# Kernel optimization log

Measured on AMD Instinct MI355X. Metric: run time of the kernel, lower is better.

## Reference

```python
import jax, jax.numpy as jnp
import numpy as np

B, R, T = 128, 36, 40
E, V, H1, H2, PH, VOC = 1024, 2048, 1024, 1024, 256, 10000


def _lstm_cell(x, h, c, Wi, Wh, b):
    # torch gate order: i, f, g, o
    g = x @ Wi.T + h @ Wh.T + b
    i, f, gg, o = jnp.split(g, 4, axis=-1)
    c_new = jax.nn.sigmoid(f) * c + jax.nn.sigmoid(i) * jnp.tanh(gg)
    h_new = jax.nn.sigmoid(o) * jnp.tanh(c_new)
    return h_new, c_new


def setup_inputs() -> dict:
    key = jax.random.key(0)
    ks = jax.random.split(key, 20)
    s = 0.05
    Vmat = jax.random.normal(ks[0], (B, R, V), jnp.float32)
    enc_features = jax.random.normal(ks[1], (B, V), jnp.float32)
    union_vfeats = jax.random.normal(ks[2], (B, V), jnp.float32)
    captions = jax.random.randint(ks[3], (B, T), 0, VOC, jnp.int32)
    lengths = jax.random.randint(ks[4], (B,), 1, T + 1, jnp.int32)
    lengths = jnp.sort(lengths)[::-1].at[0].set(T)  # sorted descending, max first
    embed_W = jax.random.normal(ks[5], (VOC, E), jnp.float32) * s
    Wi1 = jax.random.normal(ks[6], (4 * H1, H2 + V + E), jnp.float32) * s
    Wh1 = jax.random.normal(ks[7], (4 * H1, H1), jnp.float32) * s
    b1 = jax.random.normal(ks[8], (4 * H1,), jnp.float32) * s
    Wi2 = jax.random.normal(ks[9], (4 * H2, H1 + V), jnp.float32) * s
    Wh2 = jax.random.normal(ks[10], (4 * H2, H2), jnp.float32) * s
    b2 = jax.random.normal(ks[11], (4 * H2,), jnp.float32) * s
    Wva = jax.random.normal(ks[12], (PH, V), jnp.float32) * s
    bva = jax.random.normal(ks[13], (PH,), jnp.float32) * s
    Wha = jax.random.normal(ks[14], (PH, H1), jnp.float32) * s
    bha = jax.random.normal(ks[15], (PH,), jnp.float32) * s
    wa = jax.random.normal(ks[16], (PH,), jnp.float32) * s
    ba = jax.random.normal(ks[17], (), jnp.float32) * s
    Wl = jax.random.normal(ks[18], (VOC, H2), jnp.float32) * s
    bl = jax.random.normal(ks[19], (VOC,), jnp.float32) * s
    return dict(Vmat=Vmat, enc_features=enc_features, union_vfeats=union_vfeats,
                captions=captions, lengths=lengths, embed_W=embed_W,
                Wi1=Wi1, Wh1=Wh1, b1=b1, Wi2=Wi2, Wh2=Wh2, b2=b2,
                Wva=Wva, bva=bva, Wha=Wha, bha=bha, wa=wa, ba=ba, Wl=Wl, bl=bl)


def reference(Vmat, enc_features, union_vfeats, captions, lengths, embed_W,
              Wi1, Wh1, b1, Wi2, Wh2, b2, Wva, bva, Wha, bha, wa, ba, Wl, bl):
    embeddings = embed_W[captions]                      # [B, T, E]
    Va = Vmat @ Wva.T + bva                             # [B, R, PH] (precompute, step-invariant)

    def step(carry, xs):
        h1, c1, h2, c2 = carry
        emb_t, i = xs
        active = (lengths > i)[:, None]                 # [B, 1]
        x1 = jnp.concatenate([h2, union_vfeats, emb_t], axis=-1)
        h1n, c1n = _lstm_cell(x1, h1, c1, Wi1, Wh1, b1)
        # top-down attention over R regions
        logit = jnp.tanh(Va + (h1n @ Wha.T + bha)[:, None, :]) @ wa + ba  # [B, R]
        atten = jax.nn.softmax(logit, axis=1)
        av = jnp.einsum('br,brd->bd', atten, Vmat)      # [B, V]
        x2 = jnp.concatenate([av, h1n], axis=-1)
        h2n, c2n = _lstm_cell(x2, h2, c2, Wi2, Wh2, b2)
        logits = h2n @ Wl.T + bl                        # [B, VOC]
        # state freeze + zero outputs for finished sequences (ragged masking)
        h1 = jnp.where(active, h1n, h1); c1 = jnp.where(active, c1n, c1)
        h2 = jnp.where(active, h2n, h2); c2 = jnp.where(active, c2n, c2)
        out_t = jnp.where(active, logits, 0.0)
        return (h1, c1, h2, c2), out_t

    z1 = jnp.zeros((B, H1), jnp.float32)
    z2 = jnp.zeros((B, H2), jnp.float32)
    xs = (jnp.transpose(embeddings, (1, 0, 2)), jnp.arange(T, dtype=jnp.int32))
    _, outs = jax.lax.scan(step, (z1, z1, z2, z2), xs)  # [T, B, VOC]
    return jnp.transpose(outs, (1, 0, 2))               # [B, T, VOC]
```

## Files before the change

### kernel.cpp

```cpp
#include <hip/hip_runtime.h>

#define EPI_PART 0
#define EPI_BF16D 1

#define T_ 40
#define VOC_ 10000

typedef __attribute__((ext_vector_type(8))) short bf16x8;
typedef __attribute__((ext_vector_type(4))) short short4v;
typedef __attribute__((ext_vector_type(8))) short short8v;
typedef __attribute__((ext_vector_type(4))) float float4v;
typedef __attribute__((ext_vector_type(4))) float f32x4;

__device__ __forceinline__ float bf2f(short s) {
  unsigned u = ((unsigned)(unsigned short)s) << 16;
  float f; __builtin_memcpy(&f, &u, 4); return f;
}
__device__ __forceinline__ short f2bf(float f) {
  unsigned u; __builtin_memcpy(&u, &f, 4);
  u += 0x7FFFu + ((u >> 16) & 1u);
  return (short)(u >> 16);
}
__device__ __forceinline__ float sigm(float x) { return 1.f / (1.f + expf(-x)); }

__device__ __forceinline__ size_t pkidx(int row, int k, int K) {
  return (size_t)(row >> 4) * 16 * K + (size_t)(k >> 3) * 128 + (size_t)((row & 15) * 8 + (k & 7));
}


__global__ __launch_bounds__(256) void k_f2bf_split(const float* __restrict__ s,
    short* __restrict__ dh, short* __restrict__ dl, long n4) {
  long i = (long)blockIdx.x * 256 + threadIdx.x;
  long stride = (long)gridDim.x * 256;
  for (; i < n4; i += stride) {
    float4v f = ((const float4v*)s)[i];
    short4v oh, ol;
    #pragma unroll
    for (int j = 0; j < 4; j++) {
      short h = f2bf(f[j]); oh[j] = h; ol[j] = f2bf(f[j] - bf2f(h));
    }
    ((short4v*)dh)[i] = oh;
    ((short4v*)dl)[i] = ol;
  }
}

__global__ __launch_bounds__(256) void k_permpk(short* __restrict__ dh, short* __restrict__ dl,
    const float* __restrict__ s1, int ld1, int col0, int K1,
    const float* __restrict__ s2, int ld2, int Ktot) {
  int K4 = Ktot >> 2;
  long n4 = 4096L * K4;
  long stride = (long)gridDim.x * 256;
  for (long i = (long)blockIdx.x * 256 + threadIdx.x; i < n4; i += stride) {
    int p = (int)(i / K4);
    int c = ((int)(i % K4)) << 2;
    int orig = ((p & 3) << 10) + (p >> 2);
    const float* src = (c < K1) ? (s1 + (long)orig * ld1 + col0 + c)
                                : (s2 + (long)orig * ld2 + (c - K1));
    float4v f = *(const float4v*)src;
    short4v oh, ol;
    #pragma unroll
    for (int j = 0; j < 4; j++) {
      short h = f2bf(f[j]); oh[j] = h; ol[j] = f2bf(f[j] - bf2f(h));
    }
    size_t d = pkidx(p, c, Ktot);
    *(short4v*)&dh[d] = oh;
    if (dl) *(short4v*)&dl[d] = ol;
  }
}

__global__ __launch_bounds__(256) void k_packpk(short* __restrict__ dh, short* __restrict__ dl,
    const float* __restrict__ src, int ld, int Nr, int Nsrc, int K) {
  int K4 = K >> 2;
  long n4 = (long)Nr * K4;
  long stride = (long)gridDim.x * 256;
  for (long i = (long)blockIdx.x * 256 + threadIdx.x; i < n4; i += stride) {
    int row = (int)(i / K4);
    int c = ((int)(i % K4)) << 2;
    float4v f = {0.f, 0.f, 0.f, 0.f};
    if (row < Nsrc) f = *(const float4v*)(src + (long)row * ld + c);
    short4v oh, ol;
    #pragma unroll
    for (int j = 0; j < 4; j++) {
      short h = f2bf(f[j]); oh[j] = h; ol[j] = f2bf(f[j] - bf2f(h));
    }
    size_t d = pkidx(row, c, K);
    *(short4v*)&dh[d] = oh;
    if (dl) *(short4v*)&dl[d] = ol;
  }
}

__global__ __launch_bounds__(256) void k_perm_bias(float* __restrict__ d1, const float* __restrict__ s1,
                                                   float* __restrict__ d2, const float* __restrict__ s2) {
  int p = blockIdx.x * 256 + threadIdx.x;
  if (p < 4096) {
    int orig = ((p & 3) << 10) + (p >> 2);
    d1[p] = s1[orig];
    d2[p] = s2[orig];
  }
}

__global__ __launch_bounds__(256) void k_gather_emb(short* __restrict__ dst, const float* __restrict__ embW,
                                                    const int* __restrict__ cap) {
  int i = blockIdx.x * 256 + threadIdx.x;
  if (i >= 5120 * 128) return;
  int row = i >> 7, c8 = (i & 127) << 3;
  int tok = cap[row];
  const float4v* s = (const float4v*)(embW + (long)tok * 1024 + c8);
  float4v f0 = s[0], f1 = s[1];
  short8v o;
  #pragma unroll
  for (int j = 0; j < 4; j++) { o[j] = f2bf(f0[j]); o[4 + j] = f2bf(f1[j]); }
  *(short8v*)(dst + (long)row * 1024 + c8) = o;
}

__global__ __launch_bounds__(256) void k_pack_whaf(float* __restrict__ dst, const float* __restrict__ Wha) {
  int i = blockIdx.x * 256 + threadIdx.x;
  int hb = i >> 8, ph = i & 255;
  float4v a = *(const float4v*)(Wha + (long)ph * 1024 + hb * 8);
  float4v b4 = *(const float4v*)(Wha + (long)ph * 1024 + hb * 8 + 4);
  *(float4v*)(dst + ((long)hb * 256 + ph) * 8) = a;
  *(float4v*)(dst + ((long)hb * 256 + ph) * 8 + 4) = b4;
}


template<int NCS, bool SA, bool SW, int EPI>
__device__ __forceinline__ void gemm_body(short* sh, int bx, int ks, int mb,
    const short* __restrict__ A, const short* __restrict__ Alo, int lda,
    const short* __restrict__ W, const short* __restrict__ Wlo, int K,
    int Npad, int Mtot, float* __restrict__ part, short* __restrict__ outbf) {
  const int tid = threadIdx.x;
  const int l = tid & 63, w = tid >> 6;
  const int rif = l & 15, kg = l >> 4;
  const int n0 = bx * 128;
  const int k0 = ks * NCS * 64;
  const int mbase = mb * 128;

  f32x4 acc[8][2];
  #pragma unroll
  for (int m = 0; m < 8; m++) {
    acc[m][0] = (f32x4){0.f, 0.f, 0.f, 0.f};
    acc[m][1] = (f32x4){0.f, 0.f, 0.f, 0.f};
  }

  bf16x8 wh[2][2][2], wl[2][2][2];
  size_t wt0 = (size_t)(n0 / 16 + w * 2) * 16 * K + (size_t)l * 8;
  size_t wt1 = wt0 + (size_t)16 * K;
  auto loadW = [&](int c, int slot) {
    size_t base = (size_t)((k0 + c * 64) >> 3) * 128;
    #pragma unroll
    for (int sk = 0; sk < 2; sk++) {
      wh[slot][sk][0] = *(const bf16x8*)(W + wt0 + base + sk * 512);
      wh[slot][sk][1] = *(const bf16x8*)(W + wt1 + base + sk * 512);
      if (SW) {
        wl[slot][sk][0] = *(const bf16x8*)(Wlo + wt0 + base + sk * 512);
        wl[slot][sk][1] = *(const bf16x8*)(Wlo + wt1 + base + sk * 512);
      }
    }
  };

  short8v rA[4], rL[4];
  const int srow = tid >> 3;
  const int scol = (tid & 7) * 8;
  auto ldA = [&](int c) {
    #pragma unroll
    for (int j = 0; j < 4; j++) {
      size_t g = (size_t)(mbase + j * 32 + srow) * lda + k0 + c * 64 + scol;
      rA[j] = *(const short8v*)(A + g);
      if (SA) rL[j] = *(const short8v*)(Alo + g);
    }
  };
  auto stA = [&]() {
    #pragma unroll
    for (int j = 0; j < 4; j++) {
      int row = j * 32 + srow;
      int idx = row * 64 + (scol ^ ((row & 7) << 3));
      *(short8v*)&sh[idx] = rA[j];
      if (SA) *(short8v*)&sh[8192 + idx] = rL[j];
    }
  };
  auto compute = [&](int slot) {
    #pragma unroll
    for (int sk = 0; sk < 2; sk++) {
      int colb = ((sk * 32 + kg * 8) ^ ((rif & 7) << 3));
      #pragma unroll
      for (int m = 0; m < 8; m++) {
        int idx = (m * 16 + rif) * 64 + colb;
        bf16x8 ah = *(const bf16x8*)&sh[idx];
        bf16x8 al;
        if (SA) al = *(const bf16x8*)&sh[8192 + idx];
        #pragma unroll
        for (int nf = 0; nf < 2; nf++) {
          acc[m][nf] = __builtin_amdgcn_mfma_f32_16x16x32_bf16(ah, wh[slot][sk][nf], acc[m][nf], 0, 0, 0);
          if (SA) acc[m][nf] = __builtin_amdgcn_mfma_f32_16x16x32_bf16(al, wh[slot][sk][nf], acc[m][nf], 0, 0, 0);
          if (SW) acc[m][nf] = __builtin_amdgcn_mfma_f32_16x16x32_bf16(ah, wl[slot][sk][nf], acc[m][nf], 0, 0, 0);
        }
      }
    }
  };

  ldA(0); loadW(0, 0);
  stA();
  __syncthreads();
  #pragma unroll
  for (int c = 0; c < NCS; c++) {
    if (c + 1 < NCS) { ldA(c + 1); loadW(c + 1, (c + 1) & 1); }
    compute(c & 1);
    __syncthreads();
    if (c + 1 < NCS) { stA(); __syncthreads(); }
  }

  #pragma unroll
  for (int nf = 0; nf < 2; nf++) {
    int colw = n0 + (w * 2 + nf) * 16 + rif;
    #pragma unroll
    for (int m = 0; m < 8; m++) {
      #pragma unroll
      for (int j = 0; j < 4; j++) {
        int row = m * 16 + kg * 4 + j;
        if constexpr (EPI == EPI_PART) {
          part[((size_t)ks * Mtot + mbase + row) * Npad + colw] = acc[m][nf][j];
        } else {
          outbf[(size_t)(mbase + row) * Npad + colw] = f2bf(acc[m][nf][j]);
        }
      }
    }
  }
}

template<int NCS, bool SA, bool SW, int EPI>
__global__ __launch_bounds__(256) void k_g6(
    const short* __restrict__ A, const short* __restrict__ Alo, int lda,
    const short* __restrict__ W, const short* __restrict__ Wlo, int K,
    int Npad, int Mtot, float* __restrict__ part, short* __restrict__ outbf) {
  __shared__ short sh[SA ? 16384 : 8192];
  gemm_body<NCS, SA, SW, EPI>(sh, blockIdx.x, blockIdx.y, blockIdx.z,
      A, Alo, lda, W, Wlo, K, Npad, Mtot, part, outbf);
}

__global__ __launch_bounds__(256) void k_sum(const float* __restrict__ part,
    float* __restrict__ out, const float* __restrict__ bias,
    long n4, int N4, int KS, long stride4) {
  long i = (long)blockIdx.x * 256 + threadIdx.x;
  if (i >= n4) return;
  float4v a = *(const float4v*)&bias[(i % N4) * 4];
  for (int s = 0; s < KS; s++) {
    float4v p = ((const float4v*)part)[s * stride4 + i];
    #pragma unroll
    for (int j = 0; j < 4; j++) a[j] += p[j];
  }
  ((float4v*)out)[i] = a;
}

__global__ __launch_bounds__(256) void k_epi2(
    const float* __restrict__ part, const float* __restrict__ b2p,
    float* __restrict__ cstate,
    const short* __restrict__ xcur_hi, const short* __restrict__ xcur_lo,
    short* __restrict__ xnext_hi, short* __restrict__ xnext_lo,
    short* __restrict__ h2n_hi, short* __restrict__ h2n_lo,
    const int* __restrict__ lengths, int t) {
  int i = blockIdx.x * 256 + threadIdx.x;
  int b = i >> 10, h = i & 1023;
  float4v g = *(const float4v*)&b2p[h * 4];
  #pragma unroll
  for (int s = 0; s < 16; s++) {
    float4v p = *(const float4v*)&part[((size_t)s * 128 + b) * 4096 + h * 4];
    #pragma unroll
    for (int j = 0; j < 4; j++) g[j] += p[j];
  }
  float co = cstate[b * 1024 + h];
  float cn = sigm(g[1]) * co + sigm(g[0]) * tanhf(g[2]);
  float hn = sigm(g[3]) * tanhf(cn);
  bool act = lengths[b] > t;
  cstate[b * 1024 + h] = act ? cn : co;
  short hi16 = f2bf(hn);
  short lo16 = f2bf(hn - bf2f(hi16));
  h2n_hi[b * 1024 + h] = hi16;
  h2n_lo[b * 1024 + h] = lo16;
  short oh = xcur_hi[b * 2048 + h];
  short ol = xcur_lo[b * 2048 + h];
  xnext_hi[b * 2048 + h] = act ? hi16 : oh;
  xnext_lo[b * 2048 + h] = act ? lo16 : ol;
}

__global__ __launch_bounds__(256) void k_dualA(
    const short* __restrict__ xcH, const short* __restrict__ xcL,
    const short* __restrict__ W1dHi, const short* __restrict__ W1dLo,
    float* __restrict__ partA,
    const short* __restrict__ h2nHi, const short* __restrict__ h2nLo,
    const short* __restrict__ WlPK, float* __restrict__ partLG, int t) {
  __shared__ short sh[16384];
  int bx = blockIdx.x;
  if (bx < 256) {
    if (t >= T_) return;
    gemm_body<4, true, true, EPI_PART>(sh, bx & 31, bx >> 5, 0,
        xcH, xcL, 2048, W1dHi, W1dLo, 2048, 4096, 128, partA, nullptr);
  } else {
    if (t == 0) return;
    int f = bx - 256;
    gemm_body<8, true, false, EPI_PART>(sh, f % 79, f / 79, 0,
        h2nHi, h2nLo, 1024, WlPK, nullptr, 1024, 10112, 128, partLG, nullptr);
  }
}

__global__ __launch_bounds__(256) void k_dualB(
    const float* __restrict__ partA,
    const float* __restrict__ zuv, const short* __restrict__ zemb,
    float* __restrict__ c1,
    const short* __restrict__ xcH, const short* __restrict__ xcL,
    short* __restrict__ xnH, short* __restrict__ xnL,
    short* __restrict__ x2H, short* __restrict__ x2L,
    const float* __restrict__ WhaF, const float* __restrict__ bha,
    const float* __restrict__ wa, const float* __restrict__ ba,
    const float* __restrict__ Va, const float* __restrict__ Vmat,
    const int* __restrict__ lengths,
    const float* __restrict__ partLG, const float* __restrict__ bl,
    float* __restrict__ out, int t) {
  __shared__ float h1f[1024];
  __shared__ float ha_sh[256];
  __shared__ float wa_sh[256];
  __shared__ float logit_sh[40];
  __shared__ float p_sh[40];
  const int tid = threadIdx.x;
  if (blockIdx.x >= 128) {
    if (t == 0) return;
    int id = (blockIdx.x - 128) * 256 + tid;
    if (id >= 320000) return;
    int b = id / 2500, q = (id % 2500) * 4;
    bool act = lengths[b] > (t - 1);
    float4v a = {0.f, 0.f, 0.f, 0.f};
    if (act) {
      a = *(const float4v*)&bl[q];
      #pragma unroll
      for (int s = 0; s < 2; s++) {
        float4v p = *(const float4v*)&partLG[((size_t)s * 128 + b) * 10112 + q];
        #pragma unroll
        for (int j = 0; j < 4; j++) a[j] += p[j];
      }
    }
    *(float4v*)&out[((size_t)b * T_ + (t - 1)) * VOC_ + q] = a;
    return;
  }
  if (t >= T_) return;
  const int b = blockIdx.x;
  const bool act = lengths[b] > t;
  #pragma unroll
  for (int i = 0; i < 4; i++) {
    int h = i * 256 + tid;
    float4v g = {0.f, 0.f, 0.f, 0.f};
    #pragma unroll
    for (int s = 0; s < 8; s++) {
      float4v p = *(const float4v*)&partA[((size_t)s * 128 + b) * 4096 + h * 4];
      #pragma unroll
      for (int j = 0; j < 4; j++) g[j] += p[j];
    }
    float4v z = *(const float4v*)&zuv[(size_t)b * 4096 + h * 4];
    short4v e4 = *(const short4v*)&zemb[((size_t)b * T_ + t) * 4096 + h * 4];
    #pragma unroll
    for (int j = 0; j < 4; j++) g[j] += z[j] + bf2f(e4[j]);
    float co = c1[b * 1024 + h];
    float cn = sigm(g[1]) * co + sigm(g[0]) * tanhf(g[2]);
    float hn = sigm(g[3]) * tanhf(cn);
    c1[b * 1024 + h] = act ? cn : co;
    h1f[h] = hn;
    short hi16 = f2bf(hn);
    short lo16 = f2bf(hn - bf2f(hi16));
    x2H[b * 4096 + 2048 + h] = hi16;
    x2L[b * 4096 + 2048 + h] = lo16;
    short oh = xcH[b * 2048 + 1024 + h];
    short ol = xcL[b * 2048 + 1024 + h];
    xnH[b * 2048 + 1024 + h] = act ? hi16 : oh;
    xnL[b * 2048 + 1024 + h] = act ? lo16 : ol;
    x2H[b * 4096 + 3072 + h] = xcH[b * 2048 + h];
    x2L[b * 4096 + 3072 + h] = xcL[b * 2048 + h];
  }
  wa_sh[tid] = wa[tid];
  __syncthreads();
  {
    float a = 0.f;
    const float* wp = WhaF + tid * 8;
    #pragma unroll 4
    for (int hb = 0; hb < 128; hb++) {
      float4v w0 = *(const float4v*)(wp + (size_t)hb * 2048);
      float4v w1 = *(const float4v*)(wp + (size_t)hb * 2048 + 4);
      #pragma unroll
      for (int j = 0; j < 4; j++) a += w0[j] * h1f[hb * 8 + j] + w1[j] * h1f[hb * 8 + 4 + j];
    }
    ha_sh[tid] = a + bha[tid];
  }
  __syncthreads();
  {
    const int r0 = tid >> 3, sl = tid & 7;
    const float ba0 = ba[0];
    for (int r = r0; r < 36; r += 32) {
      const float4v* va4 = (const float4v*)(Va + ((long)b * 36 + r) * 256 + sl * 32);
      float part = 0.f;
      #pragma unroll
      for (int q = 0; q < 8; q++) {
        float4v v4 = va4[q];
        #pragma unroll
        for (int j = 0; j < 4; j++) {
          int ph = sl * 32 + q * 4 + j;
          part += tanhf(v4[j] + ha_sh[ph]) * wa_sh[ph];
        }
      }
      part += __shfl_down(part, 4, 8);
      part += __shfl_down(part, 2, 8);
      part += __shfl_down(part, 1, 8);
      if (sl == 0) logit_sh[r] = part + ba0;
    }
  }
  __syncthreads();
  if (tid < 64) {
    float v = (tid < 36) ? logit_sh[tid] : -3.4e38f;
    float m = v;
    #pragma unroll
    for (int off = 32; off > 0; off >>= 1) m = fmaxf(m, __shfl_xor(m, off));
    float e = (tid < 36) ? expf(v - m) : 0.f;
    float s = e;
    #pragma unroll
    for (int off = 32; off > 0; off >>= 1) s += __shfl_xor(s, off);
    if (tid < 36) p_sh[tid] = e / s;
  }
  __syncthreads();
  {
    float av[8];
    #pragma unroll
    for (int j = 0; j < 8; j++) av[j] = 0.f;
    const float* vb = Vmat + (long)b * (36 * 2048) + tid * 8;
    for (int r = 0; r < 36; r++) {
      float p = p_sh[r];
      float4v v0 = *(const float4v*)(vb + (long)r * 2048);
      float4v v1 = *(const float4v*)(vb + (long)r * 2048 + 4);
      #pragma unroll
      for (int j = 0; j < 4; j++) { av[j] += p * v0[j]; av[4 + j] += p * v1[j]; }
    }
    short8v oh, ol;
    #pragma unroll
    for (int j = 0; j < 8; j++) {
      short h = f2bf(av[j]);
      oh[j] = h;
      ol[j] = f2bf(av[j] - bf2f(h));
    }
    *(short8v*)(x2H + b * 4096 + tid * 8) = oh;
    *(short8v*)(x2L + b * 4096 + tid * 8) = ol;
  }
}

extern "C" void kernel_launch(void* const* d_in, const int* in_sizes, int n_in,
                              void* d_out, int out_size, void* d_ws, size_t ws_size,
                              hipStream_t stream) {
  const float* Vmat = (const float*)d_in[0];
  const float* uv   = (const float*)d_in[2];
  const int* captions = (const int*)d_in[3];
  const int* lengths  = (const int*)d_in[4];
  const float* embW = (const float*)d_in[5];
  const float* Wi1 = (const float*)d_in[6];
  const float* Wh1 = (const float*)d_in[7];
  const float* b1  = (const float*)d_in[8];
  const float* Wi2 = (const float*)d_in[9];
  const float* Wh2 = (const float*)d_in[10];
  const float* b2  = (const float*)d_in[11];
  const float* Wva = (const float*)d_in[12];
  const float* bva = (const float*)d_in[13];
  const float* Wha = (const float*)d_in[14];
  const float* bha = (const float*)d_in[15];
  const float* wa  = (const float*)d_in[16];
  const float* ba  = (const float*)d_in[17];
  const float* Wl  = (const float*)d_in[18];
  const float* bl  = (const float*)d_in[19];
  (void)in_sizes; (void)n_in; (void)out_size; (void)ws_size;

  char* ws = (char*)d_ws;
  size_t off = 0;
  auto alloc = [&](size_t bytes) { void* p = ws + off; off += (bytes + 255) & ~255UL; return p; };
  short* W1dHi = (short*)alloc(4096L * 2048 * 2);
  short* W1dLo = (short*)alloc(4096L * 2048 * 2);
  short* W2dHi = (short*)alloc(4096L * 4096 * 2);
  short* W2dLo = (short*)alloc(4096L * 4096 * 2);
  short* WlPK  = (short*)alloc(10112L * 1024 * 2);
  float* WhaF  = (float*)alloc(128L * 256 * 8 * 4);
  float* VaBuf = (float*)alloc(4608L * 256 * 4);
  float* Z1uvB = (float*)alloc(128L * 4096 * 4);
  short* Z1embB = (short*)alloc(5120L * 4096 * 2);
  float* partA = (float*)alloc(16L * 128 * 4096 * 4);
  float* partLG = (float*)alloc(2L * 128 * 10112 * 4);
  float* b1P = (float*)alloc(4096 * 4);
  float* b2P = (float*)alloc(4096 * 4);
  short* x1Hi = (short*)alloc(2L * 128 * 2048 * 2);
  short* x1Lo = (short*)alloc(2L * 128 * 2048 * 2);
  short* x2Hi = (short*)alloc(128L * 4096 * 2);
  short* x2Lo = (short*)alloc(128L * 4096 * 2);
  short* h2nHi = (short*)alloc(128L * 1024 * 2);
  short* h2nLo = (short*)alloc(128L * 1024 * 2);
  float* c1 = (float*)alloc(128L * 1024 * 4);
  float* c2 = (float*)alloc(128L * 1024 * 4);

  short* W1uvHi = W2dHi;
  short* W1uvLo = W2dHi + 4096L * 2048;
  float* zuvPart = (float*)(W2dHi + 4096L * 4096);
  short* uvHi = W2dHi + 4096L * 4096 + 4096L * 2048 + 2097152;
  short* uvLo = uvHi + 128L * 2048;
  short* WvaHi = uvLo + 128L * 2048;
  short* WvaLo = WvaHi + 256L * 2048;
  float* vaPart = (float*)W2dHi;
  short* W1ePk = (short*)partA;
  short* AembBF = (short*)partA + 4096L * 1024;
  short* VmatHi = Z1embB;
  short* VmatLo = Z1embB + 4608L * 2048;

  (void)hipMemsetAsync(x1Hi, 0, 2L * 128 * 2048 * 2, stream);
  (void)hipMemsetAsync(x1Lo, 0, 2L * 128 * 2048 * 2, stream);
  (void)hipMemsetAsync(c1, 0, 128L * 1024 * 4, stream);
  (void)hipMemsetAsync(c2, 0, 128L * 1024 * 4, stream);

  k_packpk<<<2048, 256, 0, stream>>>(WlPK, nullptr, Wl, 1024, 10112, 10000, 1024);
  k_pack_whaf<<<128, 256, 0, stream>>>(WhaF, Wha);
  k_packpk<<<512, 256, 0, stream>>>(WvaHi, WvaLo, Wva, 2048, 256, 256, 2048);
  k_permpk<<<2048, 256, 0, stream>>>(W1dHi, W1dLo, Wi1, 4096, 0, 1024, Wh1, 1024, 2048);
  k_permpk<<<2048, 256, 0, stream>>>(W1uvHi, W1uvLo, Wi1, 4096, 1024, 2048, Wi1, 4096, 2048);
  k_permpk<<<1024, 256, 0, stream>>>(W1ePk, nullptr, Wi1, 4096, 3072, 1024, Wi1, 4096, 1024);
  k_perm_bias<<<16, 256, 0, stream>>>(b1P, b1, b2P, b2);
  k_gather_emb<<<2560, 256, 0, stream>>>(AembBF, embW, captions);
  k_f2bf_split<<<2048, 256, 0, stream>>>(Vmat, VmatHi, VmatLo, 128L * 36 * 2048 / 4);
  k_f2bf_split<<<64, 256, 0, stream>>>(uv, uvHi, uvLo, 128L * 2048 / 4);

  k_g6<4, true, true, EPI_PART><<<dim3(32, 8, 1), 256, 0, stream>>>(
      uvHi, uvLo, 2048, W1uvHi, W1uvLo, 2048, 4096, 128, zuvPart, nullptr);
  k_sum<<<512, 256, 0, stream>>>(zuvPart, Z1uvB, b1P, 131072, 1024, 8, 131072);
  k_g6<4, true, true, EPI_PART><<<dim3(2, 8, 36), 256, 0, stream>>>(
      VmatHi, VmatLo, 2048, WvaHi, WvaLo, 2048, 256, 4608, vaPart, nullptr);
  k_sum<<<1152, 256, 0, stream>>>(vaPart, VaBuf, bva, 294912, 64, 8, 294912);
  k_permpk<<<4096, 256, 0, stream>>>(W2dHi, W2dLo, Wi2, 3072, 0, 3072, Wh2, 1024, 4096);
  k_g6<16, false, false, EPI_BF16D><<<dim3(32, 1, 40), 256, 0, stream>>>(
      AembBF, nullptr, 1024, W1ePk, nullptr, 1024, 4096, 5120, nullptr, Z1embB);

  for (int t = 0; t <= T_; t++) {
    const short* xcH = x1Hi + (size_t)(t & 1) * (128 * 2048);
    const short* xcL = x1Lo + (size_t)(t & 1) * (128 * 2048);
    short* xnH = x1Hi + (size_t)((t + 1) & 1) * (128 * 2048);
    short* xnL = x1Lo + (size_t)((t + 1) & 1) * (128 * 2048);
    k_dualA<<<414, 256, 0, stream>>>(xcH, xcL, W1dHi, W1dLo, partA,
        h2nHi, h2nLo, WlPK, partLG, t);
    k_dualB<<<1378, 256, 0, stream>>>(partA, Z1uvB, Z1embB, c1,
        xcH, xcL, xnH, xnL, x2Hi, x2Lo, WhaF, bha, wa, ba, VaBuf, Vmat,
        lengths, partLG, bl, (float*)d_out, t);
    if (t < T_) {
      k_g6<4, true, true, EPI_PART><<<dim3(32, 16, 1), 256, 0, stream>>>(
          x2Hi, x2Lo, 4096, W2dHi, W2dLo, 4096, 4096, 128, partA, nullptr);
      k_epi2<<<512, 256, 0, stream>>>(partA, b2P, c2,
          xcH, xcL, xnH, xnL, h2nHi, h2nLo, lengths, t);
    }
  }
}
```

Before: 3.761 ms.

## Hoist LSTM2 h2-recurrent GEMM slice into dualA and process two batches per attention block

The LSTM2 GEMM's K range that depends only on h2 (the last 1024 columns of W2, fed from the previous x1 buffer) is moved into the k_dualA launch as extra blocks writing split-K slices 8-9. The remaining LSTM2 GEMM covers K=3072 with 8 splits of 6 chunks, and epi2 sums 10 partial slices instead of 16. The dualB attention blocks now handle two batch rows each, halving block count and sharing the Wha weight reads across both rows. The x2 copy of h2 is no longer written. Work shifts onto an already-running launch, at the cost of a longer dualA and lower parallelism in dualB.

```diff
diff --git a/kernel.cpp b/kernel.cpp
--- a/kernel.cpp
+++ b/kernel.cpp
@@ -127,12 +127,13 @@
 __device__ __forceinline__ void gemm_body(short* sh, int bx, int ks, int mb,
     const short* __restrict__ A, const short* __restrict__ Alo, int lda,
     const short* __restrict__ W, const short* __restrict__ Wlo, int K,
+    int kA0, int kW0, int sbase,
     int Npad, int Mtot, float* __restrict__ part, short* __restrict__ outbf) {
   const int tid = threadIdx.x;
   const int l = tid & 63, w = tid >> 6;
   const int rif = l & 15, kg = l >> 4;
   const int n0 = bx * 128;
-  const int k0 = ks * NCS * 64;
+  const int kloc = ks * NCS * 64;
   const int mbase = mb * 128;
 
   f32x4 acc[8][2];
@@ -146,7 +147,7 @@
   size_t wt0 = (size_t)(n0 / 16 + w * 2) * 16 * K + (size_t)l * 8;
   size_t wt1 = wt0 + (size_t)16 * K;
   auto loadW = [&](int c, int slot) {
-    size_t base = (size_t)((k0 + c * 64) >> 3) * 128;
+    size_t base = (size_t)((kW0 + kloc + c * 64) >> 3) * 128;
     #pragma unroll
     for (int sk = 0; sk < 2; sk++) {
       wh[slot][sk][0] = *(const bf16x8*)(W + wt0 + base + sk * 512);
@@ -164,7 +165,7 @@
   auto ldA = [&](int c) {
     #pragma unroll
     for (int j = 0; j < 4; j++) {
-      size_t g = (size_t)(mbase + j * 32 + srow) * lda + k0 + c * 64 + scol;
+      size_t g = (size_t)(mbase + j * 32 + srow) * lda + kA0 + kloc + c * 64 + scol;
       rA[j] = *(const short8v*)(A + g);
       if (SA) rL[j] = *(const short8v*)(Alo + g);
     }
@@ -218,7 +219,7 @@
       for (int j = 0; j < 4; j++) {
         int row = m * 16 + kg * 4 + j;
         if constexpr (EPI == EPI_PART) {
-          part[((size_t)ks * Mtot + mbase + row) * Npad + colw] = acc[m][nf][j];
+          part[((size_t)(sbase + ks) * Mtot + mbase + row) * Npad + colw] = acc[m][nf][j];
         } else {
           outbf[(size_t)(mbase + row) * Npad + colw] = f2bf(acc[m][nf][j]);
         }
@@ -234,7 +235,7 @@
     int Npad, int Mtot, float* __restrict__ part, short* __restrict__ outbf) {
   __shared__ short sh[SA ? 16384 : 8192];
   gemm_body<NCS, SA, SW, EPI>(sh, blockIdx.x, blockIdx.y, blockIdx.z,
-      A, Alo, lda, W, Wlo, K, Npad, Mtot, part, outbf);
+      A, Alo, lda, W, Wlo, K, 0, 0, 0, Npad, Mtot, part, outbf);
 }
 
 __global__ __launch_bounds__(256) void k_sum(const float* __restrict__ part,
@@ -262,7 +263,7 @@
   int b = i >> 10, h = i & 1023;
   float4v g = *(const float4v*)&b2p[h * 4];
   #pragma unroll
-  for (int s = 0; s < 16; s++) {
+  for (int s = 0; s < 10; s++) {
     float4v p = *(const float4v*)&part[((size_t)s * 128 + b) * 4096 + h * 4];
     #pragma unroll
     for (int j = 0; j < 4; j++) g[j] += p[j];
@@ -287,18 +288,24 @@
     const short* __restrict__ W1dHi, const short* __restrict__ W1dLo,
     float* __restrict__ partA,
     const short* __restrict__ h2nHi, const short* __restrict__ h2nLo,
-    const short* __restrict__ WlPK, float* __restrict__ partLG, int t) {
+    const short* __restrict__ WlPK, float* __restrict__ partLG,
+    const short* __restrict__ W2dHi, const short* __restrict__ W2dLo, int t) {
   __shared__ short sh[16384];
   int bx = blockIdx.x;
   if (bx < 256) {
     if (t >= T_) return;
     gemm_body<4, true, true, EPI_PART>(sh, bx & 31, bx >> 5, 0,
-        xcH, xcL, 2048, W1dHi, W1dLo, 2048, 4096, 128, partA, nullptr);
-  } else {
+        xcH, xcL, 2048, W1dHi, W1dLo, 2048, 0, 0, 0, 4096, 128, partA, nullptr);
+  } else if (bx < 414) {
     if (t == 0) return;
     int f = bx - 256;
     gemm_body<8, true, false, EPI_PART>(sh, f % 79, f / 79, 0,
-        h2nHi, h2nLo, 1024, WlPK, nullptr, 1024, 10112, 128, partLG, nullptr);
+        h2nHi, h2nLo, 1024, WlPK, nullptr, 1024, 0, 0, 0, 10112, 128, partLG, nullptr);
+  } else {
+    if (t >= T_) return;
+    int f2 = bx - 414;
+    gemm_body<8, true, true, EPI_PART>(sh, f2 & 31, f2 >> 5, 0,
+        xcH, xcL, 2048, W2dHi, W2dLo, 4096, 0, 3072, 8, 4096, 128, partA, nullptr);
   }
 }
 
@@ -315,15 +322,15 @@
     const int* __restrict__ lengths,
     const float* __restrict__ partLG, const float* __restrict__ bl,
     float* __restrict__ out, int t) {
-  __shared__ float h1f[1024];
-  __shared__ float ha_sh[256];
+  __shared__ float h1f[2048];
+  __shared__ float ha_sh[512];
   __shared__ float wa_sh[256];
-  __shared__ float logit_sh[40];
-  __shared__ float p_sh[40];
+  __shared__ float logit_sh[80];
+  __shared__ float p_sh[80];
   const int tid = threadIdx.x;
-  if (blockIdx.x >= 128) {
+  if (blockIdx.x >= 64) {
     if (t == 0) return;
-    int id = (blockIdx.x - 128) * 256 + tid;
+    int id = (blockIdx.x - 64) * 256 + tid;
     if (id >= 320000) return;
     int b = id / 2500, q = (id % 2500) * 4;
     bool act = lengths[b] > (t - 1);
@@ -341,94 +348,109 @@
     return;
   }
   if (t >= T_) return;
-  const int b = blockIdx.x;
-  const bool act = lengths[b] > t;
-  #pragma unroll
-  for (int i = 0; i < 4; i++) {
-    int h = i * 256 + tid;
-    float4v g = {0.f, 0.f, 0.f, 0.f};
-    #pragma unroll
-    for (int s = 0; s < 8; s++) {
-      float4v p = *(const float4v*)&partA[((size_t)s * 128 + b) * 4096 + h * 4];
-      #pragma unroll
-      for (int j = 0; j < 4; j++) g[j] += p[j];
-    }
-    float4v z = *(const float4v*)&zuv[(size_t)b * 4096 + h * 4];
-    short4v e4 = *(const short4v*)&zemb[((size_t)b * T_ + t) * 4096 + h * 4];
-    #pragma unroll
-    for (int j = 0; j < 4; j++) g[j] += z[j] + bf2f(e4[j]);
-    float co = c1[b * 1024 + h];
-    float cn = sigm(g[1]) * co + sigm(g[0]) * tanhf(g[2]);
-    float hn = sigm(g[3]) * tanhf(cn);
-    c1[b * 1024 + h] = act ? cn : co;
-    h1f[h] = hn;
-    short hi16 = f2bf(hn);
-    short lo16 = f2bf(hn - bf2f(hi16));
-    x2H[b * 4096 + 2048 + h] = hi16;
-    x2L[b * 4096 + 2048 + h] = lo16;
-    short oh = xcH[b * 2048 + 1024 + h];
-    short ol = xcL[b * 2048 + 1024 + h];
-    xnH[b * 2048 + 1024 + h] = act ? hi16 : oh;
-    xnL[b * 2048 + 1024 + h] = act ? lo16 : ol;
-    x2H[b * 4096 + 3072 + h] = xcH[b * 2048 + h];
-    x2L[b * 4096 + 3072 + h] = xcL[b * 2048 + h];
+  const int b0 = blockIdx.x * 2;
+  #pragma unroll
+  for (int bq = 0; bq < 2; bq++) {
+    const int b = b0 + bq;
+    const bool act = lengths[b] > t;
+    #pragma unroll
+    for (int i = 0; i < 4; i++) {
+      int h = i * 256 + tid;
+      float4v g = {0.f, 0.f, 0.f, 0.f};
+      #pragma unroll
+      for (int s = 0; s < 8; s++) {
+        float4v p = *(const float4v*)&partA[((size_t)s * 128 + b) * 4096 + h * 4];
+        #pragma unroll
+        for (int j = 0; j < 4; j++) g[j] += p[j];
+      }
+      float4v z = *(const float4v*)&zuv[(size_t)b * 4096 + h * 4];
+      short4v e4 = *(const short4v*)&zemb[((size_t)b * T_ + t) * 4096 + h * 4];
+      #pragma unroll
+      for (int j = 0; j < 4; j++) g[j] += z[j] + bf2f(e4[j]);
+      float co = c1[b * 1024 + h];
+      float cn = sigm(g[1]) * co + sigm(g[0]) * tanhf(g[2]);
+      float hn = sigm(g[3]) * tanhf(cn);
+      c1[b * 1024 + h] = act ? cn : co;
+      h1f[bq * 1024 + h] = hn;
+      short hi16 = f2bf(hn);
+      short lo16 = f2bf(hn - bf2f(hi16));
+      x2H[b * 4096 + 2048 + h] = hi16;
+      x2L[b * 4096 + 2048 + h] = lo16;
+      short oh = xcH[b * 2048 + 1024 + h];
+      short ol = xcL[b * 2048 + 1024 + h];
+      xnH[b * 2048 + 1024 + h] = act ? hi16 : oh;
+      xnL[b * 2048 + 1024 + h] = act ? lo16 : ol;
+    }
   }
   wa_sh[tid] = wa[tid];
   __syncthreads();
   {
-    float a = 0.f;
+    float a0 = 0.f, a1 = 0.f;
     const float* wp = WhaF + tid * 8;
     #pragma unroll 4
     for (int hb = 0; hb < 128; hb++) {
       float4v w0 = *(const float4v*)(wp + (size_t)hb * 2048);
       float4v w1 = *(const float4v*)(wp + (size_t)hb * 2048 + 4);
       #pragma unroll
-      for (int j = 0; j < 4; j++) a += w0[j] * h1f[hb * 8 + j] + w1[j] * h1f[hb * 8 + 4 + j];
-    }
-    ha_sh[tid] = a + bha[tid];
+      for (int j = 0; j < 4; j++) {
+        a0 += w0[j] * h1f[hb * 8 + j] + w1[j] * h1f[hb * 8 + 4 + j];
+        a1 += w0[j] * h1f[1024 + hb * 8 + j] + w1[j] * h1f[1024 + hb * 8 + 4 + j];
+      }
+    }
+    float bh = bha[tid];
+    ha_sh[tid] = a0 + bh;
+    ha_sh[256 + tid] = a1 + bh;
   }
   __syncthreads();
   {
     const int r0 = tid >> 3, sl = tid & 7;
     const float ba0 = ba[0];
-    for (int r = r0; r < 36; r += 32) {
-      const float4v* va4 = (const float4v*)(Va + ((long)b * 36 + r) * 256 + sl * 32);
-      float part = 0.f;
-      #pragma unroll
-      for (int q = 0; q < 8; q++) {
-        float4v v4 = va4[q];
+    #pragma unroll
+    for (int bq = 0; bq < 2; bq++) {
+      for (int r = r0; r < 36; r += 32) {
+        const float4v* va4 = (const float4v*)(Va + ((long)(b0 + bq) * 36 + r) * 256 + sl * 32);
+        float part = 0.f;
         #pragma unroll
-        for (int j = 0; j < 4; j++) {
-          int ph = sl * 32 + q * 4 + j;
-          part += tanhf(v4[j] + ha_sh[ph]) * wa_sh[ph];
+        for (int q = 0; q < 8; q++) {
+          float4v v4 = va4[q];
+          #pragma unroll
+          for (int j = 0; j < 4; j++) {
+            int ph = sl * 32 + q * 4 + j;
+            part += tanhf(v4[j] + ha_sh[bq * 256 + ph]) * wa_sh[ph];
+          }
         }
-      }
-      part += __shfl_down(part, 4, 8);
-      part += __shfl_down(part, 2, 8);
-      part += __shfl_down(part, 1, 8);
-      if (sl == 0) logit_sh[r] = part + ba0;
-    }
-  }
-  __syncthreads();
-  if (tid < 64) {
-    float v = (tid < 36) ? logit_sh[tid] : -3.4e38f;
-    float m = v;
-    #pragma unroll
-    for (int off = 32; off > 0; off >>= 1) m = fmaxf(m, __shfl_xor(m, off));
-    float e = (tid < 36) ? expf(v - m) : 0.f;
-    float s = e;
-    #pragma unroll
-    for (int off = 32; off > 0; off >>= 1) s += __shfl_xor(s, off);
-    if (tid < 36) p_sh[tid] = e / s;
+        part += __shfl_down(part, 4, 8);
+        part += __shfl_down(part, 2, 8);
+        part += __shfl_down(part, 1, 8);
+        if (sl == 0) logit_sh[bq * 40 + r] = part + ba0;
+      }
+    }
   }
   __syncthreads();
   {
+    int wv = tid >> 6, ln = tid & 63;
+    if (wv < 2) {
+      float v = (ln < 36) ? logit_sh[wv * 40 + ln] : -3.4e38f;
+      float m = v;
+      #pragma unroll
+      for (int o = 32; o > 0; o >>= 1) m = fmaxf(m, __shfl_xor(m, o));
+      float e = (ln < 36) ? expf(v - m) : 0.f;
+      float s = e;
+      #pragma unroll
+      for (int o = 32; o > 0; o >>= 1) s += __shfl_xor(s, o);
+      if (ln < 36) p_sh[wv * 40 + ln] = e / s;
+    }
+  }
+  __syncthreads();
+  #pragma unroll
+  for (int bq = 0; bq < 2; bq++) {
+    const int b = b0 + bq;
     float av[8];
     #pragma unroll
     for (int j = 0; j < 8; j++) av[j] = 0.f;
     const float* vb = Vmat + (long)b * (36 * 2048) + tid * 8;
     for (int r = 0; r < 36; r++) {
-      float p = p_sh[r];
+      float p = p_sh[bq * 40 + r];
       float4v v0 = *(const float4v*)(vb + (long)r * 2048);
       float4v v1 = *(const float4v*)(vb + (long)r * 2048 + 4);
       #pragma unroll
@@ -482,7 +504,7 @@
   float* VaBuf = (float*)alloc(4608L * 256 * 4);
   float* Z1uvB = (float*)alloc(128L * 4096 * 4);
   short* Z1embB = (short*)alloc(5120L * 4096 * 2);
-  float* partA = (float*)alloc(16L * 128 * 4096 * 4);
+  float* partA = (float*)alloc(10L * 128 * 4096 * 4);
   float* partLG = (float*)alloc(2L * 128 * 10112 * 4);
   float* b1P = (float*)alloc(4096 * 4);
   float* b2P = (float*)alloc(4096 * 4);
@@ -539,13 +561,13 @@
     const short* xcL = x1Lo + (size_t)(t & 1) * (128 * 2048);
     short* xnH = x1Hi + (size_t)((t + 1) & 1) * (128 * 2048);
     short* xnL = x1Lo + (size_t)((t + 1) & 1) * (128 * 2048);
-    k_dualA<<<414, 256, 0, stream>>>(xcH, xcL, W1dHi, W1dLo, partA,
-        h2nHi, h2nLo, WlPK, partLG, t);
-    k_dualB<<<1378, 256, 0, stream>>>(partA, Z1uvB, Z1embB, c1,
+    k_dualA<<<478, 256, 0, stream>>>(xcH, xcL, W1dHi, W1dLo, partA,
+        h2nHi, h2nLo, WlPK, partLG, W2dHi, W2dLo, t);
+    k_dualB<<<1314, 256, 0, stream>>>(partA, Z1uvB, Z1embB, c1,
         xcH, xcL, xnH, xnL, x2Hi, x2Lo, WhaF, bha, wa, ba, VaBuf, Vmat,
         lengths, partLG, bl, (float*)d_out, t);
     if (t < T_) {
-      k_g6<4, true, true, EPI_PART><<<dim3(32, 16, 1), 256, 0, stream>>>(
+      k_g6<6, true, true, EPI_PART><<<dim3(32, 8, 1), 256, 0, stream>>>(
           x2Hi, x2Lo, 4096, W2dHi, W2dLo, 4096, 4096, 128, partA, nullptr);
       k_epi2<<<512, 256, 0, stream>>>(partA, b2P, c2,
           xcH, xcL, xnH, xnL, h2nHi, h2nLo, lengths, t);
```

New measurement: 4.238 ms. 12.7% more time.
